# Performance work log

Hardware: AMD Instinct MI355X
Metric: run time of the kernel (lower is better)

## Reference

```python
import jax, jax.numpy as jnp
import numpy as np

B, N = 16, 4096
COORD, VAL = 2, 3
LD = 256          # latent_dim / code_dim
NC = 1024         # num_codes
HID = 256         # hidden_size
NL = 5            # num_layers
NV = 4            # num_latent_vectors (residual VQ stages)
NI = 1000         # num_images
CC = 0.25         # commitment_cost
OMEGA = 30.0


def setup_inputs() -> dict:
    key = jax.random.key(0)
    ks = jax.random.split(key, 12)
    coords = jax.random.uniform(ks[0], (B, N, COORD), jnp.float32, -1.0, 1.0)
    latent_indices = jax.random.randint(ks[1], (B,), 0, NI)
    latents = jax.random.normal(ks[2], (NI, NV, LD), jnp.float32)
    emb = jax.random.normal(ks[3], (NV, NC, LD), jnp.float32)
    emb = emb / jnp.linalg.norm(emb, axis=-1, keepdims=True)
    mod_W = jax.random.normal(ks[4], (NL, LD, 2 * HID), jnp.float32) * (1.0 / np.sqrt(LD))
    mod_b = jnp.zeros((NL, 2 * HID), jnp.float32)
    # SIREN init
    W0 = jax.random.uniform(ks[5], (COORD, HID), jnp.float32, -1.0 / COORD, 1.0 / COORD)
    b0 = jax.random.uniform(ks[6], (HID,), jnp.float32, -1.0 / np.sqrt(COORD), 1.0 / np.sqrt(COORD))
    w_bound = np.sqrt(6.0 / HID) / OMEGA
    Wh = jax.random.uniform(ks[7], (NL - 1, HID, HID), jnp.float32, -w_bound, w_bound)
    bh = jax.random.uniform(ks[8], (NL - 1, HID), jnp.float32, -1.0 / np.sqrt(HID), 1.0 / np.sqrt(HID))
    Wl = jax.random.uniform(ks[9], (HID, VAL), jnp.float32, -w_bound, w_bound)
    bl = jax.random.uniform(ks[10], (VAL,), jnp.float32, -1.0 / np.sqrt(HID), 1.0 / np.sqrt(HID))
    return {"coords": coords, "latent_indices": latent_indices, "latents": latents,
            "emb": emb, "mod_W": mod_W, "mod_b": mod_b, "W0": W0, "b0": b0,
            "Wh": Wh, "bh": bh, "Wl": Wl, "bl": bl}


def reference(coords, latent_indices, latents, emb, mod_W, mod_b, W0, b0, Wh, bh, Wl, bl):
    sg = jax.lax.stop_gradient
    # per-image latent, summed over latent vectors -> [B, LD]
    img_latents = latents[latent_indices]
    z = img_latents.sum(axis=1)
    residual = z
    z_q_sum = jnp.zeros_like(z)
    vq_loss = jnp.float32(0.0)
    for s in range(NV):  # fixed small residual-VQ stage loop
        E = emb[s]  # [NC, LD]
        # squared euclidean distances [B, NC]
        dist = (jnp.sum(residual ** 2, axis=1, keepdims=True)
                - 2.0 * residual @ E.T + jnp.sum(E ** 2, axis=1))
        idx = jnp.argmin(dist, axis=1)
        z_q = E[idx]  # [B, LD]
        z_q_st = residual + sg(z_q - residual)  # straight-through
        vq_loss = vq_loss + CC * jnp.mean((sg(z_q) - residual) ** 2)
        z_q_sum = z_q_sum + z_q_st
        residual = sg(residual - z_q_st)
    vq_loss = vq_loss / NV
    effective_z = z_q_sum  # eval: no warmup scaling
    # FiLM params per layer: [B, NL, 2*HID]
    mods = jnp.einsum('bd,ldh->blh', effective_z, mod_W) + mod_b
    gam, bet = jnp.split(mods, 2, axis=-1)  # each [B, NL, HID]
    # SIREN decoder, keeping [B, N, HID] layout
    x = jnp.sin(OMEGA * (coords @ W0 + b0))
    for i in range(1, NL):
        pre = x @ Wh[i - 1] + bh[i - 1]
        pre = pre * (1.0 + gam[:, i, None, :]) + bet[:, i, None, :]
        x = jnp.sin(OMEGA * pre)
    values = x @ Wl + bl  # [B, N, VAL]
    return values, vq_loss
```

## Files before the change

kernel.cpp:

```cpp
#include <hip/hip_runtime.h>
#include <math.h>

#define LDIM 256
#define NCODES 1024
#define HID 256
#define NLAY 5
#define NVQ 4
#define CC_ 0.25f
#define OMEGA_ 30.0f
#define BATCH 16
#define NPTS 4096
#define PTILE 128

#define WIN_OFF 4096
#define FILM_OFF 8192
#define WP_BYTE 196608
#define PLANE_SHORTS (4 * 16 * 8 * 64 * 8)
#define FAST_WS_NEEDED 1245184u

typedef __attribute__((ext_vector_type(8))) short short8;
typedef __attribute__((ext_vector_type(4))) float f32x4;

__device__ __forceinline__ unsigned int pack_split(float x) {
  unsigned int u = __builtin_bit_cast(unsigned int, x);
  float hf = __builtin_bit_cast(float, u & 0xffff0000u);
  float lf = x - hf;
  unsigned int ul = __builtin_bit_cast(unsigned int, lf);
  return (u & 0xffff0000u) | (ul >> 16);
}
__device__ __forceinline__ void split_trunc(float x, short& hi, short& lo) {
  unsigned int u = __builtin_bit_cast(unsigned int, x);
  float hf = __builtin_bit_cast(float, u & 0xffff0000u);
  float lf = x - hf;
  hi = (short)(u >> 16);
  lo = (short)(__builtin_bit_cast(unsigned int, lf) >> 16);
}
__device__ __forceinline__ float bf16_hi_f(unsigned short h) {
  return __builtin_bit_cast(float, (unsigned int)h << 16);
}
__device__ __forceinline__ unsigned int mono_u32(float f) {
  unsigned int u = __builtin_bit_cast(unsigned int, f);
  return (u & 0x80000000u) ? ~u : (u | 0x80000000u);
}

__global__ __launch_bounds__(256) void vq_init(const int* __restrict__ lidx,
                                               const float* __restrict__ latents,
                                               float* __restrict__ ws) {
  const int t = threadIdx.x, b = blockIdx.x;
  const int ib = lidx[b];
  float z = 0.f;
  #pragma unroll
  for (int v = 0; v < NVQ; ++v) z += latents[((size_t)ib * NVQ + v) * LDIM + t];
  ws[b * LDIM + t] = z;
  if (t < NVQ) ((unsigned long long*)(ws + WIN_OFF))[b * NVQ + t] = ~0ULL;
}

__global__ __launch_bounds__(256) void vq_stage(const float* __restrict__ emb,
                                                float* __restrict__ ws, int stage) {
  __shared__ __align__(16) float Ech[32 * 260];
  __shared__ __align__(16) float r_s[LDIM];
  __shared__ float mval[256];
  __shared__ int   midx[256];
  const int t = threadIdx.x;
  const int b = blockIdx.x >> 3;
  const int slice = blockIdx.x & 7;
  const unsigned long long* wsl = (const unsigned long long*)(ws + WIN_OFF);
  float r = ws[b * LDIM + t];
  for (int j = 0; j < stage; ++j) {
    int wj = (int)(wsl[b * NVQ + j] & 0xffffffffULL);
    r -= emb[((size_t)j * NCODES + wj) * LDIM + t];
  }
  r_s[t] = r;
  __syncthreads();
  const float* E = emb + (size_t)stage * NCODES * LDIM + (size_t)slice * 128 * LDIM;
  const float4* E4 = (const float4*)E;
  const int cg = t >> 3;
  const int dq = t & 7;
  float bestv = 3.4e38f; int besti = 0;
  for (int ch = 0; ch < 4; ++ch) {
    __syncthreads();
    #pragma unroll
    for (int it = 0; it < 8; ++it) {
      int f = it * 256 + t;
      int row = f >> 6;
      int col4 = f & 63;
      *(float4*)&Ech[row * 260 + col4 * 4] = E4[(size_t)(ch * 32 + row) * 64 + col4];
    }
    __syncthreads();
    float dot = 0.f, e2 = 0.f;
    const float* er = &Ech[cg * 260];
    const float4* rr4 = (const float4*)r_s;
    #pragma unroll
    for (int j = 0; j < 8; ++j) {
      int d4 = dq + 8 * j;
      float4 e = *(const float4*)&er[d4 * 4];
      float4 rv = rr4[d4];
      dot += e.x * rv.x + e.y * rv.y + e.z * rv.z + e.w * rv.w;
      e2  += e.x * e.x + e.y * e.y + e.z * e.z + e.w * e.w;
    }
    dot += __shfl_xor(dot, 1); e2 += __shfl_xor(e2, 1);
    dot += __shfl_xor(dot, 2); e2 += __shfl_xor(e2, 2);
    dot += __shfl_xor(dot, 4); e2 += __shfl_xor(e2, 4);
    if (dq == 0) {
      float dist = e2 - 2.f * dot;
      int c = slice * 128 + ch * 32 + cg;
      if (dist < bestv) { bestv = dist; besti = c; }
    }
  }
  mval[t] = (dq == 0) ? bestv : 3.4e38f;
  midx[t] = (dq == 0) ? besti : (1 << 30);
  __syncthreads();
  for (int off = 128; off > 0; off >>= 1) {
    if (t < off) {
      float ov = mval[t + off]; int oi = midx[t + off];
      if (ov < mval[t] || (ov == mval[t] && oi < midx[t])) { mval[t] = ov; midx[t] = oi; }
    }
    __syncthreads();
  }
  if (t == 0) {
    unsigned long long pack =
        ((unsigned long long)mono_u32(mval[0]) << 32) | (unsigned int)midx[0];
    atomicMin((unsigned long long*)(ws + WIN_OFF) + (b * NVQ + stage), pack);
  }
}

__global__ __launch_bounds__(256) void film_loss(const float* __restrict__ emb,
                                                 const float* __restrict__ mod_W,
                                                 const float* __restrict__ mod_b,
                                                 float* __restrict__ ws,
                                                 float* __restrict__ loss_out) {
  __shared__ float z_s[LDIM];
  const int t = threadIdx.x;
  const unsigned long long* wsl = (const unsigned long long*)(ws + WIN_OFF);
  if (blockIdx.x == 64) {
    __shared__ float red[256];
    float acc = 0.f;
    for (int b = 0; b < BATCH; ++b) {
      float r = ws[b * LDIM + t];
      #pragma unroll
      for (int s = 0; s < NVQ; ++s) {
        int w = (int)(wsl[b * NVQ + s] & 0xffffffffULL);
        float e = emb[((size_t)s * NCODES + w) * LDIM + t];
        float d = e - r;
        acc += d * d;
        r -= e;
      }
    }
    red[t] = acc;
    __syncthreads();
    for (int off = 128; off > 0; off >>= 1) {
      if (t < off) red[t] += red[t + off];
      __syncthreads();
    }
    if (t == 0) loss_out[0] = red[0] * (CC_ / (NVQ * BATCH * LDIM));
    return;
  }
  const int li = blockIdx.x & 3;
  const int b  = blockIdx.x >> 2;
  const int l  = li + 1;
  float z = 0.f;
  #pragma unroll
  for (int s = 0; s < NVQ; ++s) {
    int w = (int)(wsl[b * NVQ + s] & 0xffffffffULL);
    z += emb[((size_t)s * NCODES + w) * LDIM + t];
  }
  z_s[t] = z;
  __syncthreads();
  float m1 = mod_b[l * 2 * HID + t];
  float m2 = mod_b[l * 2 * HID + HID + t];
  const float* Wm = mod_W + (size_t)l * LDIM * 2 * HID;
  #pragma unroll 4
  for (int d = 0; d < LDIM; ++d) {
    float zd = z_s[d];
    m1 = fmaf(zd, Wm[d * 2 * HID + t], m1);
    m2 = fmaf(zd, Wm[d * 2 * HID + HID + t], m2);
  }
  float* film = ws + FILM_OFF;
  film[((b * 4 + li) * 2 + 0) * HID + t] = 1.f + m1;
  film[((b * 4 + li) * 2 + 1) * HID + t] = m2;
}

__global__ __launch_bounds__(256) void prep_w(const float* __restrict__ Whg,
                                              float* __restrict__ ws) {
  const int li = blockIdx.x >> 3;
  const int c  = blockIdx.x & 7;
  const int t = threadIdx.x;
  const int lane = t & 63;
  const int n = lane & 15, q = lane >> 4;
  short* wp_hi = (short*)((char*)ws + WP_BYTE);
  short* wp_lo = wp_hi + PLANE_SHORTS;
  for (int h_t = (t >> 6); h_t < 16; h_t += 4) {
    short8 hv, lv;
    #pragma unroll
    for (int j = 0; j < 8; ++j) {
      float x = Whg[((size_t)(li * 256 + c * 32 + q * 8 + j)) * 256 + h_t * 16 + n];
      short hi, lo;
      split_trunc(x, hi, lo);
      hv[j] = hi; lv[j] = lo;
    }
    size_t off = ((((size_t)li * 16 + h_t) * 8 + c) * 64 + lane) * 8;
    *(short8*)&wp_hi[off] = hv;
    *(short8*)&wp_lo[off] = lv;
  }
}

__global__ __launch_bounds__(512) void siren_mfma_fast(
    const float* __restrict__ coords,
    const float* __restrict__ W0,
    const float* __restrict__ b0,
    const float* __restrict__ bhv,
    const float* __restrict__ Wl,
    const float* __restrict__ bl,
    const float* __restrict__ ws,
    float* __restrict__ out) {
  __shared__ short x_h[128 * 264];
  __shared__ short x_l[128 * 264];
  __shared__ float osum[128 * 4 * 3];
  const int tid = threadIdx.x;
  const int bp = blockIdx.x;
  const int b = bp >> 5;
  const int tile = bp & 31;
  const int pbase = b * NPTS + tile * PTILE;

  {
    const int quarter = tid >> 7;
    const int p = tid & 127;
    const float c0 = coords[(size_t)(pbase + p) * 2 + 0];
    const float c1 = coords[(size_t)(pbase + p) * 2 + 1];
    const int d0 = quarter * 64;
    for (int i = 0; i < 64; i += 8) {
      short8 hv, lv;
      #pragma unroll
      for (int j = 0; j < 8; ++j) {
        int d = d0 + i + j;
        float pre = fmaf(c0, W0[d], fmaf(c1, W0[HID + d], b0[d]));
        short hi, lo;
        split_trunc(__sinf(OMEGA_ * pre), hi, lo);
        hv[j] = hi; lv[j] = lo;
      }
      *(short8*)&x_h[p * 264 + d0 + i] = hv;
      *(short8*)&x_l[p * 264 + d0 + i] = lv;
    }
  }

  const int lane = tid & 63;
  const int wv = tid >> 6;
  const int pg = wv & 1;
  const int hq = wv >> 1;
  const int pb = pg * 64;
  const int hb = hq * 64;
  const int n = lane & 15;
  const int q = lane >> 4;

  const short* wp_hi = (const short*)((const char*)ws + WP_BYTE);
  const short* wp_lo = wp_hi + PLANE_SHORTS;
  const float* film = ws + FILM_OFF;

  for (int layer = 1; layer < NLAY; ++layer) {
    const int li = layer - 1;
    f32x4 acc[4][4];
    #pragma unroll
    for (int pt = 0; pt < 4; ++pt)
      #pragma unroll
      for (int ht = 0; ht < 4; ++ht)
        acc[pt][ht] = (f32x4){0.f, 0.f, 0.f, 0.f};

    __syncthreads();

    #pragma unroll 2
    for (int kc = 0; kc < HID; kc += 32) {
      const int c = kc >> 5;
      short8 Bh[4], Bl[4];
      #pragma unroll
      for (int ht = 0; ht < 4; ++ht) {
        const size_t wb = ((((size_t)li * 16 + hq * 4 + ht) * 8 + c) * 64 + lane) * 8;
        Bh[ht] = *(const short8*)&wp_hi[wb];
        Bl[ht] = *(const short8*)&wp_lo[wb];
      }
      short8 Ah[4], Al[4];
      #pragma unroll
      for (int pt = 0; pt < 4; ++pt) {
        const int xb = (pb + pt * 16 + n) * 264 + kc + q * 8;
        Ah[pt] = *(const short8*)&x_h[xb];
        Al[pt] = *(const short8*)&x_l[xb];
      }
      #pragma unroll
      for (int ht = 0; ht < 4; ++ht)
        #pragma unroll
        for (int pt = 0; pt < 4; ++pt)
          acc[pt][ht] = __builtin_amdgcn_mfma_f32_16x16x32_bf16(Ah[pt], Bh[ht], acc[pt][ht], 0, 0, 0);
      #pragma unroll
      for (int ht = 0; ht < 4; ++ht)
        #pragma unroll
        for (int pt = 0; pt < 4; ++pt)
          acc[pt][ht] = __builtin_amdgcn_mfma_f32_16x16x32_bf16(Ah[pt], Bl[ht], acc[pt][ht], 0, 0, 0);
      #pragma unroll
      for (int ht = 0; ht < 4; ++ht)
        #pragma unroll
        for (int pt = 0; pt < 4; ++pt)
          acc[pt][ht] = __builtin_amdgcn_mfma_f32_16x16x32_bf16(Al[pt], Bh[ht], acc[pt][ht], 0, 0, 0);
    }

    __syncthreads();

    #pragma unroll
    for (int ht = 0; ht < 4; ++ht) {
      const int h = hb + ht * 16 + n;
      const float bias = bhv[li * HID + h];
      const float g1 = film[((b * 4 + li) * 2 + 0) * HID + h];
      const float bt = film[((b * 4 + li) * 2 + 1) * HID + h];
      #pragma unroll
      for (int pt = 0; pt < 4; ++pt) {
        #pragma unroll
        for (int r = 0; r < 4; ++r) {
          float pre = acc[pt][ht][r] + bias;
          pre = fmaf(pre, g1, bt);
          short hi, lo;
          split_trunc(__sinf(OMEGA_ * pre), hi, lo);
          const int row = pb + pt * 16 + q * 4 + r;
          x_h[row * 264 + h] = hi;
          x_l[row * 264 + h] = lo;
        }
      }
    }
  }
  __syncthreads();

  {
    const int p = tid >> 2;
    const int dq = tid & 3;
    float v0 = 0.f, v1 = 0.f, v2 = 0.f;
    for (int i = 0; i < 64; ++i) {
      int d = dq * 64 + i;
      float xv = bf16_hi_f((unsigned short)x_h[p * 264 + d]) +
                 bf16_hi_f((unsigned short)x_l[p * 264 + d]);
      v0 = fmaf(xv, Wl[d * 3 + 0], v0);
      v1 = fmaf(xv, Wl[d * 3 + 1], v1);
      v2 = fmaf(xv, Wl[d * 3 + 2], v2);
    }
    osum[(p * 4 + dq) * 3 + 0] = v0;
    osum[(p * 4 + dq) * 3 + 1] = v1;
    osum[(p * 4 + dq) * 3 + 2] = v2;
  }
  __syncthreads();
  if (tid < PTILE) {
    const int p = tid;
    float v[3] = {bl[0], bl[1], bl[2]};
    #pragma unroll
    for (int dq = 0; dq < 4; ++dq)
      #pragma unroll
      for (int c = 0; c < 3; ++c) v[c] += osum[(p * 4 + dq) * 3 + c];
    size_t o = (size_t)(pbase + p) * 3;
    out[o + 0] = v[0]; out[o + 1] = v[1]; out[o + 2] = v[2];
  }
}

__global__ __launch_bounds__(512) void siren_mfma(
    const float* __restrict__ coords,
    const float* __restrict__ W0,
    const float* __restrict__ b0,
    const float* __restrict__ Whg,
    const float* __restrict__ bhv,
    const float* __restrict__ Wl,
    const float* __restrict__ bl,
    const float* __restrict__ ws,
    float* __restrict__ out) {
  __shared__ unsigned int x_u[128 * 260];
  __shared__ float osum[128 * 4 * 3];
  const int tid = threadIdx.x;
  const int bp = blockIdx.x;
  const int b = bp >> 5;
  const int tile = bp & 31;
  const int pbase = b * NPTS + tile * PTILE;
  {
    const int quarter = tid >> 7;
    const int p = tid & 127;
    const float c0 = coords[(size_t)(pbase + p) * 2 + 0];
    const float c1 = coords[(size_t)(pbase + p) * 2 + 1];
    const int d0 = quarter * 64;
    for (int i = 0; i < 64; i += 4) {
      unsigned int buf[4];
      #pragma unroll
      for (int j = 0; j < 4; ++j) {
        int d = d0 + i + j;
        float pre = fmaf(c0, W0[d], fmaf(c1, W0[HID + d], b0[d]));
        buf[j] = pack_split(__sinf(OMEGA_ * pre));
      }
      *(uint4*)&x_u[p * 260 + d0 + i] = *(uint4*)buf;
    }
  }
  const int lane = tid & 63;
  const int wv = tid >> 6;
  const int pg = wv & 1;
  const int hq = wv >> 1;
  const int pb = pg * 64;
  const int hb = hq * 64;
  const int n = lane & 15;
  const int q = lane >> 4;
  const float* film = ws + FILM_OFF;
  for (int layer = 1; layer < NLAY; ++layer) {
    const int li = layer - 1;
    f32x4 acc[4][4];
    #pragma unroll
    for (int pt = 0; pt < 4; ++pt)
      #pragma unroll
      for (int ht = 0; ht < 4; ++ht)
        acc[pt][ht] = (f32x4){0.f, 0.f, 0.f, 0.f};
    __syncthreads();
    for (int kc = 0; kc < HID; kc += 32) {
      short8 Bh[4], Bl[4];
      #pragma unroll
      for (int ht = 0; ht < 4; ++ht) {
        const float* wbase = Whg + ((size_t)(li * 256 + kc + q * 8)) * 256 + hb + ht * 16 + n;
        #pragma unroll
        for (int j = 0; j < 8; ++j) {
          short hi, lo;
          split_trunc(wbase[(size_t)j * 256], hi, lo);
          Bh[ht][j] = hi; Bl[ht][j] = lo;
        }
      }
      short8 ah[4], al[4];
      #pragma unroll
      for (int pt = 0; pt < 4; ++pt) {
        const uint4* ap = (const uint4*)&x_u[(pb + pt * 16 + n) * 260 + kc + q * 8];
        uint4 a0 = ap[0], a1 = ap[1];
        unsigned int aw[8] = {a0.x, a0.y, a0.z, a0.w, a1.x, a1.y, a1.z, a1.w};
        #pragma unroll
        for (int j = 0; j < 8; ++j) {
          ah[pt][j] = (short)(aw[j] >> 16);
          al[pt][j] = (short)(aw[j] & 0xffffu);
        }
      }
      #pragma unroll
      for (int ht = 0; ht < 4; ++ht)
        #pragma unroll
        for (int pt = 0; pt < 4; ++pt)
          acc[pt][ht] = __builtin_amdgcn_mfma_f32_16x16x32_bf16(ah[pt], Bh[ht], acc[pt][ht], 0, 0, 0);
      #pragma unroll
      for (int ht = 0; ht < 4; ++ht)
        #pragma unroll
        for (int pt = 0; pt < 4; ++pt)
          acc[pt][ht] = __builtin_amdgcn_mfma_f32_16x16x32_bf16(ah[pt], Bl[ht], acc[pt][ht], 0, 0, 0);
      #pragma unroll
      for (int ht = 0; ht < 4; ++ht)
        #pragma unroll
        for (int pt = 0; pt < 4; ++pt)
          acc[pt][ht] = __builtin_amdgcn_mfma_f32_16x16x32_bf16(al[pt], Bh[ht], acc[pt][ht], 0, 0, 0);
    }
    __syncthreads();
    #pragma unroll
    for (int ht = 0; ht < 4; ++ht) {
      const int h = hb + ht * 16 + n;
      const float bias = bhv[li * HID + h];
      const float g1 = film[((b * 4 + li) * 2 + 0) * HID + h];
      const float bt = film[((b * 4 + li) * 2 + 1) * HID + h];
      #pragma unroll
      for (int pt = 0; pt < 4; ++pt) {
        #pragma unroll
        for (int r = 0; r < 4; ++r) {
          float pre = acc[pt][ht][r] + bias;
          pre = fmaf(pre, g1, bt);
          x_u[(pb + pt * 16 + q * 4 + r) * 260 + h] = pack_split(__sinf(OMEGA_ * pre));
        }
      }
    }
  }
  __syncthreads();
  {
    const int p = tid >> 2;
    const int dq = tid & 3;
    float v0 = 0.f, v1 = 0.f, v2 = 0.f;
    for (int i = 0; i < 64; ++i) {
      int d = dq * 64 + i;
      unsigned int wrd = x_u[p * 260 + d];
      float xv = bf16_hi_f((unsigned short)(wrd >> 16)) +
                 bf16_hi_f((unsigned short)(wrd & 0xffffu));
      v0 = fmaf(xv, Wl[d * 3 + 0], v0);
      v1 = fmaf(xv, Wl[d * 3 + 1], v1);
      v2 = fmaf(xv, Wl[d * 3 + 2], v2);
    }
    osum[(p * 4 + dq) * 3 + 0] = v0;
    osum[(p * 4 + dq) * 3 + 1] = v1;
    osum[(p * 4 + dq) * 3 + 2] = v2;
  }
  __syncthreads();
  if (tid < PTILE) {
    const int p = tid;
    float v[3] = {bl[0], bl[1], bl[2]};
    #pragma unroll
    for (int dq = 0; dq < 4; ++dq)
      #pragma unroll
      for (int c = 0; c < 3; ++c) v[c] += osum[(p * 4 + dq) * 3 + c];
    size_t o = (size_t)(pbase + p) * 3;
    out[o + 0] = v[0]; out[o + 1] = v[1]; out[o + 2] = v[2];
  }
}

extern "C" void kernel_launch(void* const* d_in, const int* in_sizes, int n_in,
                              void* d_out, int out_size, void* d_ws, size_t ws_size,
                              hipStream_t stream) {
  (void)in_sizes; (void)n_in;
  const float* coords  = (const float*)d_in[0];
  const int*   lidx    = (const int*)d_in[1];
  const float* latents = (const float*)d_in[2];
  const float* emb     = (const float*)d_in[3];
  const float* mod_W   = (const float*)d_in[4];
  const float* mod_b   = (const float*)d_in[5];
  const float* W0      = (const float*)d_in[6];
  const float* b0      = (const float*)d_in[7];
  const float* Wh      = (const float*)d_in[8];
  const float* bh      = (const float*)d_in[9];
  const float* Wl      = (const float*)d_in[10];
  const float* bl      = (const float*)d_in[11];
  float* out = (float*)d_out;
  float* ws  = (float*)d_ws;
  float* loss_out = out + (out_size - 1);

  const bool fast = (ws_size >= FAST_WS_NEEDED);
  if (fast) prep_w<<<32, 256, 0, stream>>>(Wh, ws);
  vq_init<<<BATCH, 256, 0, stream>>>(lidx, latents, ws);
  for (int s = 0; s < NVQ; ++s)
    vq_stage<<<BATCH * 8, 256, 0, stream>>>(emb, ws, s);
  film_loss<<<BATCH * 4 + 1, 256, 0, stream>>>(emb, mod_W, mod_b, ws, loss_out);
  if (fast)
    siren_mfma_fast<<<(BATCH * NPTS) / PTILE, 512, 0, stream>>>(coords, W0, b0, bh, Wl, bl, ws, out);
  else
    siren_mfma<<<(BATCH * NPTS) / PTILE, 512, 0, stream>>>(coords, W0, b0, Wh, bh, Wl, bl, ws, out);
}
```

Baseline: 256.6 us.

## Fuse VQ stages into one kernel and halve SIREN point tile

Replaces the init kernel and the four per-stage VQ launches with one kernel per batch item that loops over all stages and updates the residual in shared memory, removing launches and global atomics. Each VQ block now scans all 1024 codes serially with 16 blocks instead of 128, which reduces parallelism on that phase. Separately, the SIREN fast kernel tile shrinks from 128 to 64 points per block, doubling the block count, cutting LDS use per block and changing the wave-to-output mapping. The smaller tile raises occupancy but halves weight-fragment reuse per block.

```diff
diff --git a/kernel.cpp b/kernel.cpp
--- a/kernel.cpp
+++ b/kernel.cpp
@@ -10,7 +10,7 @@
 #define OMEGA_ 30.0f
 #define BATCH 16
 #define NPTS 4096
-#define PTILE 128
+#define PTILE 64
 
 #define WIN_OFF 4096
 #define FILM_OFF 8192
@@ -38,89 +38,82 @@
 __device__ __forceinline__ float bf16_hi_f(unsigned short h) {
   return __builtin_bit_cast(float, (unsigned int)h << 16);
 }
-__device__ __forceinline__ unsigned int mono_u32(float f) {
-  unsigned int u = __builtin_bit_cast(unsigned int, f);
-  return (u & 0x80000000u) ? ~u : (u | 0x80000000u);
-}
-
-__global__ __launch_bounds__(256) void vq_init(const int* __restrict__ lidx,
-                                               const float* __restrict__ latents,
-                                               float* __restrict__ ws) {
-  const int t = threadIdx.x, b = blockIdx.x;
-  const int ib = lidx[b];
-  float z = 0.f;
-  #pragma unroll
-  for (int v = 0; v < NVQ; ++v) z += latents[((size_t)ib * NVQ + v) * LDIM + t];
-  ws[b * LDIM + t] = z;
-  if (t < NVQ) ((unsigned long long*)(ws + WIN_OFF))[b * NVQ + t] = ~0ULL;
-}
-
-__global__ __launch_bounds__(256) void vq_stage(const float* __restrict__ emb,
-                                                float* __restrict__ ws, int stage) {
-  __shared__ __align__(16) float Ech[32 * 260];
+
+__global__ __launch_bounds__(512) void vq_all(const int* __restrict__ lidx,
+                                              const float* __restrict__ latents,
+                                              const float* __restrict__ emb,
+                                              float* __restrict__ ws) {
+  __shared__ __align__(16) float Ech[64 * 260];
   __shared__ __align__(16) float r_s[LDIM];
-  __shared__ float mval[256];
-  __shared__ int   midx[256];
+  __shared__ float mval[64];
+  __shared__ int   midx[64];
   const int t = threadIdx.x;
-  const int b = blockIdx.x >> 3;
-  const int slice = blockIdx.x & 7;
-  const unsigned long long* wsl = (const unsigned long long*)(ws + WIN_OFF);
-  float r = ws[b * LDIM + t];
-  for (int j = 0; j < stage; ++j) {
-    int wj = (int)(wsl[b * NVQ + j] & 0xffffffffULL);
-    r -= emb[((size_t)j * NCODES + wj) * LDIM + t];
-  }
-  r_s[t] = r;
+  const int b = blockIdx.x;
+  const int lane = t & 63;
+  const int wv = t >> 6;
+  const int cg = lane >> 3;
+  const int dq = lane & 7;
+  const int c_local = wv * 8 + cg;
+
+  if (t < LDIM) {
+    const int ib = lidx[b];
+    float z = 0.f;
+    #pragma unroll
+    for (int v = 0; v < NVQ; ++v) z += latents[((size_t)ib * NVQ + v) * LDIM + t];
+    ws[b * LDIM + t] = z;
+    r_s[t] = z;
+  }
   __syncthreads();
-  const float* E = emb + (size_t)stage * NCODES * LDIM + (size_t)slice * 128 * LDIM;
-  const float4* E4 = (const float4*)E;
-  const int cg = t >> 3;
-  const int dq = t & 7;
-  float bestv = 3.4e38f; int besti = 0;
-  for (int ch = 0; ch < 4; ++ch) {
-    __syncthreads();
-    #pragma unroll
-    for (int it = 0; it < 8; ++it) {
-      int f = it * 256 + t;
-      int row = f >> 6;
-      int col4 = f & 63;
-      *(float4*)&Ech[row * 260 + col4 * 4] = E4[(size_t)(ch * 32 + row) * 64 + col4];
-    }
-    __syncthreads();
-    float dot = 0.f, e2 = 0.f;
-    const float* er = &Ech[cg * 260];
-    const float4* rr4 = (const float4*)r_s;
-    #pragma unroll
-    for (int j = 0; j < 8; ++j) {
-      int d4 = dq + 8 * j;
-      float4 e = *(const float4*)&er[d4 * 4];
-      float4 rv = rr4[d4];
-      dot += e.x * rv.x + e.y * rv.y + e.z * rv.z + e.w * rv.w;
-      e2  += e.x * e.x + e.y * e.y + e.z * e.z + e.w * e.w;
-    }
-    dot += __shfl_xor(dot, 1); e2 += __shfl_xor(e2, 1);
-    dot += __shfl_xor(dot, 2); e2 += __shfl_xor(e2, 2);
-    dot += __shfl_xor(dot, 4); e2 += __shfl_xor(e2, 4);
-    if (dq == 0) {
-      float dist = e2 - 2.f * dot;
-      int c = slice * 128 + ch * 32 + cg;
-      if (dist < bestv) { bestv = dist; besti = c; }
-    }
-  }
-  mval[t] = (dq == 0) ? bestv : 3.4e38f;
-  midx[t] = (dq == 0) ? besti : (1 << 30);
-  __syncthreads();
-  for (int off = 128; off > 0; off >>= 1) {
-    if (t < off) {
-      float ov = mval[t + off]; int oi = midx[t + off];
-      if (ov < mval[t] || (ov == mval[t] && oi < midx[t])) { mval[t] = ov; midx[t] = oi; }
-    }
-    __syncthreads();
-  }
-  if (t == 0) {
-    unsigned long long pack =
-        ((unsigned long long)mono_u32(mval[0]) << 32) | (unsigned int)midx[0];
-    atomicMin((unsigned long long*)(ws + WIN_OFF) + (b * NVQ + stage), pack);
+
+  for (int s = 0; s < NVQ; ++s) {
+    const float* E = emb + (size_t)s * NCODES * LDIM;
+    const float4* E4 = (const float4*)E;
+    float bestv = 3.4e38f; int besti = 0;
+    for (int ch = 0; ch < 16; ++ch) {
+      __syncthreads();
+      #pragma unroll
+      for (int it = 0; it < 8; ++it) {
+        int f = it * 512 + t;
+        int row = f >> 6;
+        int col4 = f & 63;
+        *(float4*)&Ech[row * 260 + col4 * 4] = E4[(size_t)(ch * 64 + row) * 64 + col4];
+      }
+      __syncthreads();
+      const float* er = &Ech[c_local * 260];
+      const float4* rr4 = (const float4*)r_s;
+      float dot = 0.f, e2 = 0.f;
+      #pragma unroll
+      for (int j = 0; j < 8; ++j) {
+        int d4 = dq + 8 * j;
+        float4 e = *(const float4*)&er[d4 * 4];
+        float4 rv = rr4[d4];
+        dot += e.x * rv.x + e.y * rv.y + e.z * rv.z + e.w * rv.w;
+        e2  += e.x * e.x + e.y * e.y + e.z * e.z + e.w * e.w;
+      }
+      dot += __shfl_xor(dot, 1); e2 += __shfl_xor(e2, 1);
+      dot += __shfl_xor(dot, 2); e2 += __shfl_xor(e2, 2);
+      dot += __shfl_xor(dot, 4); e2 += __shfl_xor(e2, 4);
+      if (dq == 0) {
+        float dist = e2 - 2.f * dot;
+        int c = ch * 64 + c_local;
+        if (dist < bestv) { bestv = dist; besti = c; }
+      }
+    }
+    __syncthreads();
+    if (dq == 0) { mval[c_local] = bestv; midx[c_local] = besti; }
+    __syncthreads();
+    for (int off = 32; off > 0; off >>= 1) {
+      if (t < off) {
+        float ov = mval[t + off]; int oi = midx[t + off];
+        if (ov < mval[t] || (ov == mval[t] && oi < midx[t])) { mval[t] = ov; midx[t] = oi; }
+      }
+      __syncthreads();
+    }
+    const int best = midx[0];
+    if (t < LDIM) r_s[t] -= E[(size_t)best * LDIM + t];
+    if (t == 0)
+      ((unsigned long long*)(ws + WIN_OFF))[b * NVQ + s] = (unsigned long long)(unsigned int)best;
+    __syncthreads();
   }
 }
 
@@ -213,22 +206,22 @@
     const float* __restrict__ bl,
     const float* __restrict__ ws,
     float* __restrict__ out) {
-  __shared__ short x_h[128 * 264];
-  __shared__ short x_l[128 * 264];
-  __shared__ float osum[128 * 4 * 3];
+  __shared__ short x_h[PTILE * 264];
+  __shared__ short x_l[PTILE * 264];
+  __shared__ float osum[PTILE * 8 * 3];
   const int tid = threadIdx.x;
   const int bp = blockIdx.x;
-  const int b = bp >> 5;
-  const int tile = bp & 31;
+  const int b = bp >> 6;
+  const int tile = bp & 63;
   const int pbase = b * NPTS + tile * PTILE;
 
   {
-    const int quarter = tid >> 7;
-    const int p = tid & 127;
+    const int oct = tid >> 6;
+    const int p = tid & 63;
     const float c0 = coords[(size_t)(pbase + p) * 2 + 0];
     const float c1 = coords[(size_t)(pbase + p) * 2 + 1];
-    const int d0 = quarter * 64;
-    for (int i = 0; i < 64; i += 8) {
+    const int d0 = oct * 32;
+    for (int i = 0; i < 32; i += 8) {
       short8 hv, lv;
       #pragma unroll
       for (int j = 0; j < 8; ++j) {
@@ -244,11 +237,8 @@
   }
 
   const int lane = tid & 63;
-  const int wv = tid >> 6;
-  const int pg = wv & 1;
-  const int hq = wv >> 1;
-  const int pb = pg * 64;
-  const int hb = hq * 64;
+  const int hq = tid >> 6;
+  const int hb = hq * 32;
   const int n = lane & 15;
   const int q = lane >> 4;
 
@@ -258,11 +248,11 @@
 
   for (int layer = 1; layer < NLAY; ++layer) {
     const int li = layer - 1;
-    f32x4 acc[4][4];
+    f32x4 acc[4][2];
     #pragma unroll
     for (int pt = 0; pt < 4; ++pt)
       #pragma unroll
-      for (int ht = 0; ht < 4; ++ht)
+      for (int ht = 0; ht < 2; ++ht)
         acc[pt][ht] = (f32x4){0.f, 0.f, 0.f, 0.f};
 
     __syncthreads();
@@ -270,32 +260,32 @@
     #pragma unroll 2
     for (int kc = 0; kc < HID; kc += 32) {
       const int c = kc >> 5;
-      short8 Bh[4], Bl[4];
-      #pragma unroll
-      for (int ht = 0; ht < 4; ++ht) {
-        const size_t wb = ((((size_t)li * 16 + hq * 4 + ht) * 8 + c) * 64 + lane) * 8;
+      short8 Bh[2], Bl[2];
+      #pragma unroll
+      for (int ht = 0; ht < 2; ++ht) {
+        const size_t wb = ((((size_t)li * 16 + hq * 2 + ht) * 8 + c) * 64 + lane) * 8;
         Bh[ht] = *(const short8*)&wp_hi[wb];
         Bl[ht] = *(const short8*)&wp_lo[wb];
       }
       short8 Ah[4], Al[4];
       #pragma unroll
       for (int pt = 0; pt < 4; ++pt) {
-        const int xb = (pb + pt * 16 + n) * 264 + kc + q * 8;
+        const int xb = (pt * 16 + n) * 264 + kc + q * 8;
         Ah[pt] = *(const short8*)&x_h[xb];
         Al[pt] = *(const short8*)&x_l[xb];
       }
       #pragma unroll
-      for (int ht = 0; ht < 4; ++ht)
+      for (int ht = 0; ht < 2; ++ht)
         #pragma unroll
         for (int pt = 0; pt < 4; ++pt)
           acc[pt][ht] = __builtin_amdgcn_mfma_f32_16x16x32_bf16(Ah[pt], Bh[ht], acc[pt][ht], 0, 0, 0);
       #pragma unroll
-      for (int ht = 0; ht < 4; ++ht)
+      for (int ht = 0; ht < 2; ++ht)
         #pragma unroll
         for (int pt = 0; pt < 4; ++pt)
           acc[pt][ht] = __builtin_amdgcn_mfma_f32_16x16x32_bf16(Ah[pt], Bl[ht], acc[pt][ht], 0, 0, 0);
       #pragma unroll
-      for (int ht = 0; ht < 4; ++ht)
+      for (int ht = 0; ht < 2; ++ht)
         #pragma unroll
         for (int pt = 0; pt < 4; ++pt)
           acc[pt][ht] = __builtin_amdgcn_mfma_f32_16x16x32_bf16(Al[pt], Bh[ht], acc[pt][ht], 0, 0, 0);
@@ -304,7 +294,7 @@
     __syncthreads();
 
     #pragma unroll
-    for (int ht = 0; ht < 4; ++ht) {
+    for (int ht = 0; ht < 2; ++ht) {
       const int h = hb + ht * 16 + n;
       const float bias = bhv[li * HID + h];
       const float g1 = film[((b * 4 + li) * 2 + 0) * HID + h];
@@ -317,7 +307,7 @@
           pre = fmaf(pre, g1, bt);
           short hi, lo;
           split_trunc(__sinf(OMEGA_ * pre), hi, lo);
-          const int row = pb + pt * 16 + q * 4 + r;
+          const int row = pt * 16 + q * 4 + r;
           x_h[row * 264 + h] = hi;
           x_l[row * 264 + h] = lo;
         }
@@ -327,29 +317,29 @@
   __syncthreads();
 
   {
-    const int p = tid >> 2;
-    const int dq = tid & 3;
+    const int p = tid >> 3;
+    const int dq = tid & 7;
     float v0 = 0.f, v1 = 0.f, v2 = 0.f;
-    for (int i = 0; i < 64; ++i) {
-      int d = dq * 64 + i;
+    for (int i = 0; i < 32; ++i) {
+      int d = dq * 32 + i;
       float xv = bf16_hi_f((unsigned short)x_h[p * 264 + d]) +
                  bf16_hi_f((unsigned short)x_l[p * 264 + d]);
       v0 = fmaf(xv, Wl[d * 3 + 0], v0);
       v1 = fmaf(xv, Wl[d * 3 + 1], v1);
       v2 = fmaf(xv, Wl[d * 3 + 2], v2);
     }
-    osum[(p * 4 + dq) * 3 + 0] = v0;
-    osum[(p * 4 + dq) * 3 + 1] = v1;
-    osum[(p * 4 + dq) * 3 + 2] = v2;
+    osum[(p * 8 + dq) * 3 + 0] = v0;
+    osum[(p * 8 + dq) * 3 + 1] = v1;
+    osum[(p * 8 + dq) * 3 + 2] = v2;
   }
   __syncthreads();
   if (tid < PTILE) {
     const int p = tid;
     float v[3] = {bl[0], bl[1], bl[2]};
     #pragma unroll
-    for (int dq = 0; dq < 4; ++dq)
-      #pragma unroll
-      for (int c = 0; c < 3; ++c) v[c] += osum[(p * 4 + dq) * 3 + c];
+    for (int dq = 0; dq < 8; ++dq)
+      #pragma unroll
+      for (int c = 0; c < 3; ++c) v[c] += osum[(p * 8 + dq) * 3 + c];
     size_t o = (size_t)(pbase + p) * 3;
     out[o + 0] = v[0]; out[o + 1] = v[1]; out[o + 2] = v[2];
   }
@@ -371,7 +361,7 @@
   const int bp = blockIdx.x;
   const int b = bp >> 5;
   const int tile = bp & 31;
-  const int pbase = b * NPTS + tile * PTILE;
+  const int pbase = b * NPTS + tile * 128;
   {
     const int quarter = tid >> 7;
     const int p = tid & 127;
@@ -484,7 +474,7 @@
     osum[(p * 4 + dq) * 3 + 2] = v2;
   }
   __syncthreads();
-  if (tid < PTILE) {
+  if (tid < 128) {
     const int p = tid;
     float v[3] = {bl[0], bl[1], bl[2]};
     #pragma unroll
@@ -518,12 +508,10 @@
 
   const bool fast = (ws_size >= FAST_WS_NEEDED);
   if (fast) prep_w<<<32, 256, 0, stream>>>(Wh, ws);
-  vq_init<<<BATCH, 256, 0, stream>>>(lidx, latents, ws);
-  for (int s = 0; s < NVQ; ++s)
-    vq_stage<<<BATCH * 8, 256, 0, stream>>>(emb, ws, s);
+  vq_all<<<BATCH, 512, 0, stream>>>(lidx, latents, emb, ws);
   film_loss<<<BATCH * 4 + 1, 256, 0, stream>>>(emb, mod_W, mod_b, ws, loss_out);
   if (fast)
     siren_mfma_fast<<<(BATCH * NPTS) / PTILE, 512, 0, stream>>>(coords, W0, b0, bh, Wl, bl, ws, out);
   else
-    siren_mfma<<<(BATCH * NPTS) / PTILE, 512, 0, stream>>>(coords, W0, b0, Wh, bh, Wl, bl, ws, out);
-}
+    siren_mfma<<<(BATCH * NPTS) / 128, 512, 0, stream>>>(coords, W0, b0, Wh, bh, Wl, bl, ws, out);
+}
```

Result: slower. 321.8 us (+25.4%).
